# Optimization experiments

Measured on AMD Instinct MI355X. Metric: run time of the kernel, lower is better.

## Reference

```python
import jax, jax.numpy as jnp
import numpy as np


def setup_inputs() -> dict:
    key = jax.random.key(0)
    ks = jax.random.split(key, 4)
    B, T, M, E, F = 4, 2048, 1024, 8, 4096
    hidden_states = jax.random.normal(ks[0], (B, T, M), dtype=jnp.float32)
    wg = jax.random.normal(ks[1], (M, E), dtype=jnp.float32) * (1.0 / np.sqrt(M))
    w1 = jax.random.normal(ks[2], (E, M, F), dtype=jnp.float32) * (1.0 / np.sqrt(M))
    b1 = jnp.zeros((E, F), dtype=jnp.float32)
    w2 = jax.random.normal(ks[3], (E, F, M), dtype=jnp.float32) * (1.0 / np.sqrt(F))
    b2 = jnp.zeros((E, M), dtype=jnp.float32)
    return {"hidden_states": hidden_states, "wg": wg, "w1": w1, "b1": b1, "w2": w2, "b2": b2}


def reference(hidden_states, wg, w1, b1, w2, b2):
    B, T, M = hidden_states.shape
    E = wg.shape[1]
    S = B * T
    MIN_CAPACITY = 4
    C = max((S + E - 1) // E, MIN_CAPACITY)  # capacity_factor = 1 (static)

    x = hidden_states.reshape(S, M)  # [S, M]

    # --- top-1 gating (deepspeed TopKGate, noisy=None, use_rts=False) ---
    logits = x @ wg                                  # [S, E]
    gates = jax.nn.softmax(logits, axis=-1)          # [S, E]
    idx = jnp.argmax(gates, axis=-1)                 # [S]
    mask1 = jax.nn.one_hot(idx, E, dtype=gates.dtype)  # [S, E]
    # aux loss (computed before capacity drop)
    l_aux = jnp.sum(gates.mean(0) * mask1.mean(0)) * E
    # position of each token within its expert's queue
    locations1 = jnp.cumsum(mask1, axis=0) - 1.0     # [S, E]
    mask1 = mask1 * (locations1 < C)                 # drop overflow tokens
    gates1_s = jnp.sum(gates * mask1, axis=1)        # [S]
    loc_s = jnp.sum(locations1 * mask1, axis=1).astype(jnp.int32)  # [S]
    loc_sc = jax.nn.one_hot(loc_s, C, dtype=gates.dtype)           # [S, C]

    combine_weights = jnp.einsum('se,sc->sec', gates1_s[:, None] * mask1, loc_sc)  # [S,E,C]
    dispatch_mask = (combine_weights > 0).astype(x.dtype)

    # --- dispatch ---
    dispatched = jnp.einsum('sec,sm->ecm', dispatch_mask, x)  # [E, C, M]

    # --- expert FFN (grouped GEMM) ---
    h = jax.nn.gelu(jnp.einsum('ecm,emf->ecf', dispatched, w1) + b1[:, None, :])
    expert_out = jnp.einsum('ecf,efm->ecm', h, w2) + b2[:, None, :]  # [E, C, M]

    # --- combine ---
    out = jnp.einsum('sec,ecm->sm', combine_weights, expert_out)  # [S, M]
    return out.reshape(B, T, M)
```

## Files before the change

### kernel.cpp

```cpp
#include <hip/hip_runtime.h>
#include <hip/hip_bf16.h>
#include <math.h>

#define S_TOK 8192
#define M_DIM 1024
#define E_NUM 8
#define F_DIM 4096
#define CAP   1024

typedef short short8 __attribute__((ext_vector_type(8)));
typedef float f32x4 __attribute__((ext_vector_type(4)));
typedef unsigned short ushortx4 __attribute__((ext_vector_type(4)));

__device__ inline unsigned short f2bf(float f) {
    union { float f; unsigned int u; } v; v.f = f;
    unsigned int r = v.u + 0x7fffu + ((v.u >> 16) & 1u);
    return (unsigned short)(r >> 16);
}

__device__ inline float gelu_fast(float x) {
    float y = 0.7978845608028654f * (x + 0.044715f * x * x * x);
    if (y > 40.f) return x;
    float e = exp2f(2.8853900817779268f * y);
    return x * e / (e + 1.0f);
}

__device__ inline void gl_lds16(const void* g, void* l) {
    __builtin_amdgcn_global_load_lds(
        (const __attribute__((address_space(1))) unsigned int*)g,
        (__attribute__((address_space(3))) unsigned int*)l, 16, 0, 0);
}

__global__ __launch_bounds__(256) void gating_kernel(
    const float* __restrict__ x, const float* __restrict__ wg,
    int* __restrict__ idx, float* __restrict__ gate)
{
    int wid = threadIdx.x >> 6;
    int lane = threadIdx.x & 63;
    int s = blockIdx.x * 4 + wid;
    const float* xs = x + (size_t)s * M_DIM;

    double acc[E_NUM];
#pragma unroll
    for (int e = 0; e < E_NUM; e++) acc[e] = 0.0;

    for (int i = lane; i < M_DIM; i += 64) {
        float xv = xs[i];
        float4 wa = *(const float4*)(wg + (size_t)i * E_NUM);
        float4 wb = *(const float4*)(wg + (size_t)i * E_NUM + 4);
        acc[0] += (double)xv * (double)wa.x;
        acc[1] += (double)xv * (double)wa.y;
        acc[2] += (double)xv * (double)wa.z;
        acc[3] += (double)xv * (double)wa.w;
        acc[4] += (double)xv * (double)wb.x;
        acc[5] += (double)xv * (double)wb.y;
        acc[6] += (double)xv * (double)wb.z;
        acc[7] += (double)xv * (double)wb.w;
    }
#pragma unroll
    for (int e = 0; e < E_NUM; e++) {
        double v = acc[e];
        for (int o = 32; o > 0; o >>= 1) v += __shfl_down(v, o, 64);
        acc[e] = v;
    }
    if (lane == 0) {
        double mx = acc[0]; int am = 0;
#pragma unroll
        for (int e = 1; e < E_NUM; e++) {
            if (acc[e] > mx) { mx = acc[e]; am = e; }
        }
        double se = 0.0;
#pragma unroll
        for (int e = 0; e < E_NUM; e++) se += exp(acc[e] - mx);
        idx[s] = am;
        gate[s] = (float)(1.0 / se);
    }
}

__global__ __launch_bounds__(1024) void scan_build(
    const int* __restrict__ idx, int* __restrict__ srcmap)
{
    __shared__ unsigned int sc[2][4][1024];
    int t = threadIdx.x;

    for (int i = t; i < E_NUM * CAP; i += 1024) srcmap[i] = -1;

    int eid[8];
    unsigned int cnt[E_NUM];
#pragma unroll
    for (int e = 0; e < E_NUM; e++) cnt[e] = 0;
#pragma unroll
    for (int i = 0; i < 8; i++) {
        int e = idx[t * 8 + i];
        eid[i] = e;
        cnt[e]++;
    }
    unsigned int pk[4];
#pragma unroll
    for (int i = 0; i < 4; i++) pk[i] = cnt[2 * i] | (cnt[2 * i + 1] << 16);
#pragma unroll
    for (int i = 0; i < 4; i++) sc[0][i][t] = pk[i];

    int buf = 0;
    for (int ofs = 1; ofs < 1024; ofs <<= 1) {
        __syncthreads();
        unsigned int v[4];
#pragma unroll
        for (int i = 0; i < 4; i++) {
            v[i] = sc[buf][i][t] + ((t >= ofs) ? sc[buf][i][t - ofs] : 0u);
            sc[buf ^ 1][i][t] = v[i];
        }
        buf ^= 1;
    }
    __syncthreads();
    unsigned int pos[E_NUM];
#pragma unroll
    for (int e = 0; e < E_NUM; e++) {
        unsigned int incl = (sc[buf][e >> 1][t] >> ((e & 1) * 16)) & 0xffffu;
        pos[e] = incl - cnt[e];
    }
#pragma unroll
    for (int i = 0; i < 8; i++) {
        int e = eid[i];
        unsigned int p = pos[e]++;
        if (p < CAP) srcmap[e * CAP + p] = t * 8 + i;
    }
}

__global__ __launch_bounds__(256) void dispatch_kernel(
    const float* __restrict__ x, const int* __restrict__ srcmap,
    unsigned short* __restrict__ A1)
{
    int slot = blockIdx.x;
    int s = srcmap[slot];
    int t = threadIdx.x;
    ushortx4 o;
    if (s >= 0) {
        float4 v = ((const float4*)(x + (size_t)s * M_DIM))[t];
        o[0] = f2bf(v.x); o[1] = f2bf(v.y); o[2] = f2bf(v.z); o[3] = f2bf(v.w);
    } else {
        o[0] = 0; o[1] = 0; o[2] = 0; o[3] = 0;
    }
    ((ushortx4*)(A1 + (size_t)slot * M_DIM))[t] = o;
}

__global__ __launch_bounds__(256) void transpose_cvt(
    const float* __restrict__ in, unsigned short* __restrict__ out, int R, int Cc)
{
    __shared__ float tile[32][33];
    int e = blockIdx.z;
    int br = blockIdx.y * 32, bc = blockIdx.x * 32;
    const float* ine = in + (size_t)e * R * Cc;
    unsigned short* oute = out + (size_t)e * R * Cc;
    int tx = threadIdx.x, ty = threadIdx.y;
#pragma unroll
    for (int i = 0; i < 32; i += 8)
        tile[ty + i][tx] = ine[(size_t)(br + ty + i) * Cc + (bc + tx)];
    __syncthreads();
#pragma unroll
    for (int i = 0; i < 32; i += 8)
        oute[(size_t)(bc + ty + i) * R + (br + tx)] = f2bf(tile[tx][ty + i]);
}

template <int MODE>
__global__ __launch_bounds__(256) void gemm_bf16(
    const unsigned short* __restrict__ A, const unsigned short* __restrict__ B,
    const float* __restrict__ bias, float* __restrict__ OutF,
    unsigned short* __restrict__ OutH,
    const int* __restrict__ srcmap, const float* __restrict__ gate,
    int K, int RA, int NB, int tilesM, int tilesN)
{
    __shared__ __align__(16) unsigned short As[2][128 * 32];
    __shared__ __align__(16) unsigned short Bs[2][128 * 32];

    int bid = blockIdx.x;
    int tpe = tilesM * tilesN;
    int e = bid / tpe;
    int rem = bid - e * tpe;
    int tm = rem / tilesN;
    int tn = rem - tm * tilesN;

    const unsigned short* Ae = A + ((size_t)e * RA + (size_t)tm * 128) * K;
    const unsigned short* Be = B + ((size_t)e * NB + (size_t)tn * 128) * K;

    int tid = threadIdx.x;
    int wid = tid >> 6, lane = tid & 63;
    int srow = wid * 32 + (lane >> 2);
    int schunk = (lane & 3) * 8;

    int fr = lane & 15, fk = (lane >> 4) * 8;
    int r0 = (wid >> 1) * 64, c0 = (wid & 1) * 64;

#define STAGE(bufi, kk) do {                                                  \
    const unsigned short* ga = Ae + (size_t)srow * K + (kk) + schunk;         \
    const unsigned short* gb = Be + (size_t)srow * K + (kk) + schunk;         \
    gl_lds16(ga,                 &As[bufi][srow * 32 + schunk]);              \
    gl_lds16(ga + (size_t)16 * K, &As[bufi][(srow + 16) * 32 + schunk]);      \
    gl_lds16(gb,                 &Bs[bufi][srow * 32 + schunk]);              \
    gl_lds16(gb + (size_t)16 * K, &Bs[bufi][(srow + 16) * 32 + schunk]);      \
} while (0)

    f32x4 acc[4][4];
#pragma unroll
    for (int i = 0; i < 4; i++)
#pragma unroll
        for (int j = 0; j < 4; j++) acc[i][j] = (f32x4){0.f, 0.f, 0.f, 0.f};

    STAGE(0, 0);
    asm volatile("s_waitcnt vmcnt(0)" ::: "memory");
    __syncthreads();

    int cur = 0;
    for (int k0 = 0; k0 < K; k0 += 32) {
        if (k0 + 32 < K) STAGE(cur ^ 1, k0 + 32);

        short8 a[4], b[4];
#pragma unroll
        for (int mi = 0; mi < 4; mi++)
            a[mi] = *(const short8*)&As[cur][(r0 + mi * 16 + fr) * 32 + fk];
#pragma unroll
        for (int ni = 0; ni < 4; ni++)
            b[ni] = *(const short8*)&Bs[cur][(c0 + ni * 16 + fr) * 32 + fk];
#pragma unroll
        for (int mi = 0; mi < 4; mi++)
#pragma unroll
            for (int ni = 0; ni < 4; ni++)
                acc[mi][ni] = __builtin_amdgcn_mfma_f32_16x16x32_bf16(
                    a[mi], b[ni], acc[mi][ni], 0, 0, 0);

        asm volatile("s_waitcnt vmcnt(0)" ::: "memory");
        __syncthreads();
        cur ^= 1;
    }
#undef STAGE

    int orow = (lane >> 4) * 4, ocol = lane & 15;
    if (MODE == 0) {
#pragma unroll
        for (int mi = 0; mi < 4; mi++) {
#pragma unroll
            for (int j = 0; j < 4; j++) {
                int r = tm * 128 + r0 + mi * 16 + orow + j;
                size_t rowbase = ((size_t)e * RA + r) * NB;
#pragma unroll
                for (int ni = 0; ni < 4; ni++) {
                    int c = tn * 128 + c0 + ni * 16 + ocol;
                    float v = acc[mi][ni][j] + bias[e * NB + c];
                    OutH[rowbase + c] = f2bf(gelu_fast(v));
                }
            }
        }
    } else {
#pragma unroll
        for (int mi = 0; mi < 4; mi++) {
#pragma unroll
            for (int j = 0; j < 4; j++) {
                int r = tm * 128 + r0 + mi * 16 + orow + j;
                int slot = e * RA + r;
                int s = srcmap[slot];
                if (s < 0) continue;
                float g = gate[s];
                size_t rowbase = (size_t)s * NB;
#pragma unroll
                for (int ni = 0; ni < 4; ni++) {
                    int c = tn * 128 + c0 + ni * 16 + ocol;
                    OutF[rowbase + c] = g * (acc[mi][ni][j] + bias[e * NB + c]);
                }
            }
        }
    }
}

extern "C" void kernel_launch(void* const* d_in, const int* in_sizes, int n_in,
                              void* d_out, int out_size, void* d_ws, size_t ws_size,
                              hipStream_t stream) {
    const float* x  = (const float*)d_in[0];
    const float* wg = (const float*)d_in[1];
    const float* w1 = (const float*)d_in[2];
    const float* b1 = (const float*)d_in[3];
    const float* w2 = (const float*)d_in[4];
    const float* b2 = (const float*)d_in[5];
    float* out = (float*)d_out;

    char* ws = (char*)d_ws;
    unsigned short* A1  = (unsigned short*)(ws);
    unsigned short* W1T = (unsigned short*)(ws + (size_t)(16u << 20));
    unsigned short* W2T = (unsigned short*)(ws + (size_t)(80u << 20));
    unsigned short* H   = (unsigned short*)(ws + (size_t)(144u << 20));
    int*   idx  = (int*)(ws + (size_t)(208u << 20));
    float* gate = (float*)(ws + (size_t)(208u << 20) + 32768);
    int*   srcm = (int*)(ws + (size_t)(208u << 20) + 65536);

    hipMemsetAsync(d_out, 0, (size_t)S_TOK * M_DIM * sizeof(float), stream);

    gating_kernel<<<S_TOK / 4, 256, 0, stream>>>(x, wg, idx, gate);
    scan_build<<<1, 1024, 0, stream>>>(idx, srcm);
    dispatch_kernel<<<E_NUM * CAP, 256, 0, stream>>>(x, srcm, A1);
    transpose_cvt<<<dim3(F_DIM / 32, M_DIM / 32, E_NUM), dim3(32, 8), 0, stream>>>(
        w1, W1T, M_DIM, F_DIM);
    transpose_cvt<<<dim3(M_DIM / 32, F_DIM / 32, E_NUM), dim3(32, 8), 0, stream>>>(
        w2, W2T, F_DIM, M_DIM);

    gemm_bf16<0><<<E_NUM * (CAP / 128) * (F_DIM / 128), 256, 0, stream>>>(
        A1, W1T, b1, nullptr, H, nullptr, nullptr,
        M_DIM, CAP, F_DIM, CAP / 128, F_DIM / 128);

    gemm_bf16<1><<<E_NUM * (CAP / 128) * (M_DIM / 128), 256, 0, stream>>>(
        H, W2T, b2, out, nullptr, srcm, gate,
        F_DIM, CAP, M_DIM, CAP / 128, M_DIM / 128);
}
```

Baseline: 375.8 us.

## Rewrite expert GEMMs with 256-row tiles, 8-phase pipelined LDS staging and swizzle

Replaces the 128x128, K=32 double-buffered GEMM with a 512-thread kernel using 256xBN tiles and K=64 steps. Loads are split into eight interleaved phases that overlap with MFMA sub-blocks, using XOR-swizzled LDS, setprio around MFMAs and an XCD-aware block swizzle. The first GEMM's epilogue is staged through LDS for coalesced 16-byte stores. This aims to raise MFMA utilization and cut LDS bank conflicts and barrier stalls. The costs are a larger LDS footprint, one block per CU, and fewer workgroups for the second GEMM (256).

```diff
diff --git a/kernel.cpp b/kernel.cpp
--- a/kernel.cpp
+++ b/kernel.cpp
@@ -163,109 +163,208 @@
 }
 
 template <int MODE>
-__global__ __launch_bounds__(256) void gemm_bf16(
+__global__ __launch_bounds__(512, 1) void gemm8p(
     const unsigned short* __restrict__ A, const unsigned short* __restrict__ B,
-    const float* __restrict__ bias, float* __restrict__ OutF,
-    unsigned short* __restrict__ OutH,
-    const int* __restrict__ srcmap, const float* __restrict__ gate,
-    int K, int RA, int NB, int tilesM, int tilesN)
+    const float* __restrict__ bias, unsigned short* __restrict__ OutH,
+    float* __restrict__ OutF, const int* __restrict__ srcmap,
+    const float* __restrict__ gate)
 {
-    __shared__ __align__(16) unsigned short As[2][128 * 32];
-    __shared__ __align__(16) unsigned short Bs[2][128 * 32];
+    constexpr int K     = (MODE == 0) ? 1024 : 4096;
+    constexpr int NB    = (MODE == 0) ? 4096 : 1024;
+    constexpr int BN    = (MODE == 0) ? 256 : 128;
+    constexpr int NT    = K / 64;
+    constexpr int TNn   = NB / BN;
+    constexpr int NWG   = E_NUM * 4 * TNn;
+    constexpr int NI    = BN / 64;
+    constexpr int NIH   = NI / 2;
+    constexpr int WN    = BN / 4;
+    constexpr int AELEM = 256 * 64;
+    constexpr int BELEM = BN * 64;
+    constexpr int BOFF  = 2 * AELEM;
+
+    __shared__ __align__(16) unsigned short LDS[BOFF + 2 * BELEM];
 
     int bid = blockIdx.x;
-    int tpe = tilesM * tilesN;
-    int e = bid / tpe;
-    int rem = bid - e * tpe;
-    int tm = rem / tilesN;
-    int tn = rem - tm * tilesN;
-
-    const unsigned short* Ae = A + ((size_t)e * RA + (size_t)tm * 128) * K;
-    const unsigned short* Be = B + ((size_t)e * NB + (size_t)tn * 128) * K;
-
-    int tid = threadIdx.x;
-    int wid = tid >> 6, lane = tid & 63;
-    int srow = wid * 32 + (lane >> 2);
-    int schunk = (lane & 3) * 8;
-
-    int fr = lane & 15, fk = (lane >> 4) * 8;
-    int r0 = (wid >> 1) * 64, c0 = (wid & 1) * 64;
-
-#define STAGE(bufi, kk) do {                                                  \
-    const unsigned short* ga = Ae + (size_t)srow * K + (kk) + schunk;         \
-    const unsigned short* gb = Be + (size_t)srow * K + (kk) + schunk;         \
-    gl_lds16(ga,                 &As[bufi][srow * 32 + schunk]);              \
-    gl_lds16(ga + (size_t)16 * K, &As[bufi][(srow + 16) * 32 + schunk]);      \
-    gl_lds16(gb,                 &Bs[bufi][srow * 32 + schunk]);              \
-    gl_lds16(gb + (size_t)16 * K, &Bs[bufi][(srow + 16) * 32 + schunk]);      \
+    int swz = (bid & 7) * (NWG / 8) + (bid >> 3);
+    int e, tm, tn;
+    {
+        int per_e = 4 * TNn;
+        e = swz / per_e;
+        int rem = swz % per_e;
+        tn = rem >> 2;
+        tm = rem & 3;
+    }
+
+    const unsigned short* Ae = A + ((size_t)e * CAP + (size_t)tm * 256) * K;
+    const unsigned short* Be = B + ((size_t)e * NB + (size_t)tn * BN) * K;
+
+    int tid = threadIdx.x, w = tid >> 6, lane = tid & 63;
+    int wm = w >> 2, wn = w & 3;
+    int fr = lane & 15, kq = lane >> 4;
+
+    int lr = lane >> 3;
+    int lc8 = (lane & 7) ^ lr;
+    const unsigned short *aS00, *aS01, *aS10, *aS11;
+    const unsigned short *bS00, *bS01, *bS10, *bS11;
+    int aD00, aD01, aD10, aD11, bD00, bD01, bD10, bD11;
+    aS00 = Ae + (size_t)(w * 8 + lr) * K + lc8 * 8;         aD00 = (w * 8) * 64;
+    aS01 = Ae + (size_t)(64 + w * 8 + lr) * K + lc8 * 8;    aD01 = (64 + w * 8) * 64;
+    aS10 = Ae + (size_t)(128 + w * 8 + lr) * K + lc8 * 8;   aD10 = (128 + w * 8) * 64;
+    aS11 = Ae + (size_t)(192 + w * 8 + lr) * K + lc8 * 8;   aD11 = (192 + w * 8) * 64;
+    if (MODE == 0) {
+        bS00 = Be + (size_t)(w * 8 + lr) * K + lc8 * 8;         bD00 = (w * 8) * 64;
+        bS01 = Be + (size_t)(64 + w * 8 + lr) * K + lc8 * 8;    bD01 = (64 + w * 8) * 64;
+        bS10 = Be + (size_t)(128 + w * 8 + lr) * K + lc8 * 8;   bD10 = (128 + w * 8) * 64;
+        bS11 = Be + (size_t)(192 + w * 8 + lr) * K + lc8 * 8;   bD11 = (192 + w * 8) * 64;
+    } else {
+        bS00 = Be + (size_t)(w * 8 + lr) * K + lc8 * 8;         bD00 = (w * 8) * 64;
+        bS01 = bS00;                                            bD01 = 0;
+        bS10 = Be + (size_t)(64 + w * 8 + lr) * K + lc8 * 8;    bD10 = (64 + w * 8) * 64;
+        bS11 = bS10;                                            bD11 = 0;
+    }
+
+#define STG_A(SL, H, T_) do {                                                  \
+    gl_lds16(aS##H##0 + (size_t)(T_) * 64, &LDS[(SL) * AELEM + aD##H##0]);     \
+    gl_lds16(aS##H##1 + (size_t)(T_) * 64, &LDS[(SL) * AELEM + aD##H##1]); } while (0)
+#define STG_B(SL, H, T_) do {                                                  \
+    gl_lds16(bS##H##0 + (size_t)(T_) * 64, &LDS[BOFF + (SL) * BELEM + bD##H##0]); \
+    if (MODE == 0)                                                             \
+        gl_lds16(bS##H##1 + (size_t)(T_) * 64, &LDS[BOFF + (SL) * BELEM + bD##H##1]); } while (0)
+
+    int rsw = fr & 7;
+    int swk0 = (kq ^ rsw) * 8;
+    int swk1 = ((4 + kq) ^ rsw) * 8;
+
+    short8 af[4][2];
+    short8 bf[NIH][2];
+    f32x4 acc[8][NI];
+#pragma unroll
+    for (int i = 0; i < 8; i++)
+#pragma unroll
+        for (int j = 0; j < NI; j++) acc[i][j] = (f32x4){0.f, 0.f, 0.f, 0.f};
+
+#define READ_A(TS, MH) do {                                                    \
+    _Pragma("unroll") for (int m2 = 0; m2 < 4; m2++) {                         \
+        int row_ = wm * 128 + ((MH) * 4 + m2) * 16 + fr;                       \
+        int b_ = (TS) * AELEM + row_ * 64;                                     \
+        af[m2][0] = *(const short8*)&LDS[b_ + swk0];                           \
+        af[m2][1] = *(const short8*)&LDS[b_ + swk1]; } } while (0)
+#define READ_B(TS, NH) do {                                                    \
+    _Pragma("unroll") for (int n2 = 0; n2 < NIH; n2++) {                       \
+        int row_ = wn * WN + ((NH) * NIH + n2) * 16 + fr;                      \
+        int b_ = BOFF + (TS) * BELEM + row_ * 64;                              \
+        bf[n2][0] = *(const short8*)&LDS[b_ + swk0];                           \
+        bf[n2][1] = *(const short8*)&LDS[b_ + swk1]; } } while (0)
+#define DO_MFMA(MH, NH) do {                                                   \
+    __builtin_amdgcn_s_setprio(1);                                             \
+    _Pragma("unroll") for (int m2 = 0; m2 < 4; m2++)                           \
+    _Pragma("unroll") for (int n2 = 0; n2 < NIH; n2++) {                       \
+        acc[(MH)*4+m2][(NH)*NIH+n2] = __builtin_amdgcn_mfma_f32_16x16x32_bf16( \
+            af[m2][0], bf[n2][0], acc[(MH)*4+m2][(NH)*NIH+n2], 0, 0, 0);       \
+        acc[(MH)*4+m2][(NH)*NIH+n2] = __builtin_amdgcn_mfma_f32_16x16x32_bf16( \
+            af[m2][1], bf[n2][1], acc[(MH)*4+m2][(NH)*NIH+n2], 0, 0, 0); }     \
+    __builtin_amdgcn_s_setprio(0);                                             \
 } while (0)
-
-    f32x4 acc[4][4];
-#pragma unroll
-    for (int i = 0; i < 4; i++)
-#pragma unroll
-        for (int j = 0; j < 4; j++) acc[i][j] = (f32x4){0.f, 0.f, 0.f, 0.f};
-
-    STAGE(0, 0);
-    asm volatile("s_waitcnt vmcnt(0)" ::: "memory");
-    __syncthreads();
-
-    int cur = 0;
-    for (int k0 = 0; k0 < K; k0 += 32) {
-        if (k0 + 32 < K) STAGE(cur ^ 1, k0 + 32);
-
-        short8 a[4], b[4];
-#pragma unroll
-        for (int mi = 0; mi < 4; mi++)
-            a[mi] = *(const short8*)&As[cur][(r0 + mi * 16 + fr) * 32 + fk];
-#pragma unroll
-        for (int ni = 0; ni < 4; ni++)
-            b[ni] = *(const short8*)&Bs[cur][(c0 + ni * 16 + fr) * 32 + fk];
-#pragma unroll
-        for (int mi = 0; mi < 4; mi++)
-#pragma unroll
-            for (int ni = 0; ni < 4; ni++)
-                acc[mi][ni] = __builtin_amdgcn_mfma_f32_16x16x32_bf16(
-                    a[mi], b[ni], acc[mi][ni], 0, 0, 0);
-
-        asm volatile("s_waitcnt vmcnt(0)" ::: "memory");
-        __syncthreads();
-        cur ^= 1;
-    }
-#undef STAGE
-
-    int orow = (lane >> 4) * 4, ocol = lane & 15;
+#define BAR() __builtin_amdgcn_s_barrier()
+
+    STG_A(0, 0, 0); STG_A(0, 1, 0); STG_B(0, 0, 0); STG_B(0, 1, 0);
+    STG_A(1, 0, 1);
+    asm volatile("s_waitcnt vmcnt(2)" ::: "memory");
+    BAR();
+
+#pragma unroll 1
+    for (int i = 0; i < NT / 2; ++i) {
+        const int T = 2 * i;
+        const bool g2 = (T + 2 < NT), g3 = (T + 3 < NT);
+        READ_A(0, 0); READ_B(0, 0);
+        STG_A(1, 1, T + 1);
+        DO_MFMA(0, 0);
+        BAR();
+        READ_B(0, 1);
+        STG_B(1, 0, T + 1);
+        DO_MFMA(0, 1);
+        BAR();
+        READ_A(0, 1); READ_B(0, 0);
+        STG_B(1, 1, T + 1);
+        DO_MFMA(1, 0);
+        BAR();
+        READ_B(0, 1);
+        if (g2) STG_A(0, 0, T + 2);
+        DO_MFMA(1, 1);
+        if (g2) asm volatile("s_waitcnt vmcnt(2)" ::: "memory");
+        else    asm volatile("s_waitcnt vmcnt(0)" ::: "memory");
+        BAR();
+        READ_A(1, 0); READ_B(1, 0);
+        if (g2) STG_A(0, 1, T + 2);
+        DO_MFMA(0, 0);
+        BAR();
+        READ_B(1, 1);
+        if (g2) STG_B(0, 0, T + 2);
+        DO_MFMA(0, 1);
+        BAR();
+        READ_A(1, 1); READ_B(1, 0);
+        if (g2) STG_B(0, 1, T + 2);
+        DO_MFMA(1, 0);
+        BAR();
+        READ_B(1, 1);
+        if (g3) STG_A(1, 0, T + 3);
+        DO_MFMA(1, 1);
+        if (g3) asm volatile("s_waitcnt vmcnt(2)" ::: "memory");
+        else    asm volatile("s_waitcnt vmcnt(0)" ::: "memory");
+        BAR();
+    }
+#undef STG_A
+#undef STG_B
+#undef READ_A
+#undef READ_B
+#undef DO_MFMA
+#undef BAR
+
     if (MODE == 0) {
-#pragma unroll
-        for (int mi = 0; mi < 4; mi++) {
+        unsigned short* R = (unsigned short*)LDS;
+        float bv[NI];
+#pragma unroll
+        for (int ni = 0; ni < NI; ni++)
+            bv[ni] = bias[e * NB + tn * BN + wn * WN + ni * 16 + fr];
+#pragma unroll
+        for (int mi = 0; mi < 8; mi++) {
 #pragma unroll
             for (int j = 0; j < 4; j++) {
-                int r = tm * 128 + r0 + mi * 16 + orow + j;
-                size_t rowbase = ((size_t)e * RA + r) * NB;
-#pragma unroll
-                for (int ni = 0; ni < 4; ni++) {
-                    int c = tn * 128 + c0 + ni * 16 + ocol;
-                    float v = acc[mi][ni][j] + bias[e * NB + c];
-                    OutH[rowbase + c] = f2bf(gelu_fast(v));
+                int row = wm * 128 + mi * 16 + kq * 4 + j;
+#pragma unroll
+                for (int ni = 0; ni < NI; ni++) {
+                    int col = wn * WN + ni * 16 + fr;
+                    R[row * 256 + (((col >> 3) ^ (row & 7)) << 3) + (col & 7)] =
+                        f2bf(gelu_fast(acc[mi][ni][j] + bv[ni]));
                 }
             }
         }
+        __syncthreads();
+        int row = tid >> 1, seg = tid & 1;
+        size_t gb = ((size_t)(e * CAP + tm * 256 + row)) * NB + tn * 256 + seg * 128;
+#pragma unroll
+        for (int i = 0; i < 16; i++) {
+            int chunk = seg * 16 + i;
+            *(short8*)&OutH[gb + i * 8] =
+                *(const short8*)&R[row * 256 + ((chunk ^ (row & 7)) << 3)];
+        }
     } else {
-#pragma unroll
-        for (int mi = 0; mi < 4; mi++) {
+        float bv[NI];
+#pragma unroll
+        for (int ni = 0; ni < NI; ni++)
+            bv[ni] = bias[e * NB + tn * BN + wn * WN + ni * 16 + fr];
+#pragma unroll
+        for (int mi = 0; mi < 8; mi++) {
 #pragma unroll
             for (int j = 0; j < 4; j++) {
-                int r = tm * 128 + r0 + mi * 16 + orow + j;
-                int slot = e * RA + r;
-                int s = srcmap[slot];
+                int r = tm * 256 + wm * 128 + mi * 16 + kq * 4 + j;
+                int s = srcmap[e * CAP + r];
                 if (s < 0) continue;
                 float g = gate[s];
-                size_t rowbase = (size_t)s * NB;
-#pragma unroll
-                for (int ni = 0; ni < 4; ni++) {
-                    int c = tn * 128 + c0 + ni * 16 + ocol;
-                    OutF[rowbase + c] = g * (acc[mi][ni][j] + bias[e * NB + c]);
-                }
+                float* ob = OutF + (size_t)s * NB + tn * BN + wn * WN;
+#pragma unroll
+                for (int ni = 0; ni < NI; ni++)
+                    ob[ni * 16 + fr] = g * (acc[mi][ni][j] + bv[ni]);
             }
         }
     }
@@ -301,11 +400,7 @@
     transpose_cvt<<<dim3(M_DIM / 32, F_DIM / 32, E_NUM), dim3(32, 8), 0, stream>>>(
         w2, W2T, F_DIM, M_DIM);
 
-    gemm_bf16<0><<<E_NUM * (CAP / 128) * (F_DIM / 128), 256, 0, stream>>>(
-        A1, W1T, b1, nullptr, H, nullptr, nullptr,
-        M_DIM, CAP, F_DIM, CAP / 128, F_DIM / 128);
-
-    gemm_bf16<1><<<E_NUM * (CAP / 128) * (M_DIM / 128), 256, 0, stream>>>(
-        H, W2T, b2, out, nullptr, srcm, gate,
-        F_DIM, CAP, M_DIM, CAP / 128, M_DIM / 128);
-}
+    gemm8p<0><<<512, 512, 0, stream>>>(A1, W1T, b1, H, nullptr, nullptr, nullptr);
+
+    gemm8p<1><<<256, 512, 0, stream>>>(H, W2T, b2, nullptr, out, srcm, gate);
+}
```

Result: faster. 356.0 us (-5.3%).
